# Optimization experiments

Hardware: AMD Instinct MI355X
Metric: run time of the kernel (lower is better)

The kernel has to match this reference:

```python
import jax, jax.numpy as jnp
import numpy as np
from jax import lax

B, NM, P, F, E, H, K = 32, 131072, 256, 3, 64, 4, 3
DH = E // H


def layer_norm(x, gamma, beta, eps=1e-5):
    mu = x.mean(-1, keepdims=True)
    var = ((x - mu) ** 2).mean(-1, keepdims=True)
    return (x - mu) * lax.rsqrt(var + eps) * gamma + beta


def knn_interp(x, pos_x, pos_y, k=K):
    """x: [B, Nx, F] features at pos_x [Nx, 2]; interpolate to pos_y [Ny, 2].
    Positions are shared across the batch (they are tiled in the torch code),
    so KNN indices/weights are computed once. Matches torch knn + inverse-
    squared-distance weighted scatter (uniform per-batch counts => gather form).
    """
    d2 = jnp.sum((pos_y[:, None, :] - pos_x[None, :, :]) ** 2, axis=-1)  # [Ny, Nx]
    neg_d2, idx = lax.top_k(-d2, k)                                      # [Ny, k]
    w = 1.0 / jnp.clip(-neg_d2, 1e-16)                                   # [Ny, k]
    w = lax.stop_gradient(w)  # torch computes weights under no_grad
    gathered = x[:, idx, :]                                              # [B, Ny, k, F]
    num = jnp.sum(gathered * w[None, :, :, None], axis=2)                # [B, Ny, F]
    den = jnp.sum(w, axis=1)[None, :, None]                              # [1, Ny, 1]
    return num / den


def setup_inputs() -> dict:
    key = jax.random.key(0)
    ks = jax.random.split(key, 8)
    return {
        "node_attr": jax.random.normal(ks[0], (B * NM, F), jnp.float32),
        "position_mesh": jax.random.uniform(ks[1], (NM, 2), jnp.float32),
        "position_pivotal": jax.random.uniform(ks[2], (P, 2), jnp.float32),
        "ln_gamma": jnp.ones((F,), jnp.float32),
        "ln_beta": jnp.zeros((F,), jnp.float32),
        "Wf": jax.random.normal(ks[3], (E, F), jnp.float32) * (2.0 / E) ** 0.5,
        "bf": jnp.zeros((E,), jnp.float32),
        "Wp": jax.random.normal(ks[4], (E, 2), jnp.float32) * (2.0 / E) ** 0.5,
        "bp": jnp.zeros((E,), jnp.float32),
        "in_proj_w": jax.random.normal(ks[5], (3 * E, E), jnp.float32) * (1.0 / E) ** 0.5,
        "in_proj_b": jnp.zeros((3 * E,), jnp.float32),
        "batch_size": B,
    }


def reference(node_attr, position_mesh, position_pivotal, ln_gamma, ln_beta,
              Wf, bf, Wp, bp, in_proj_w, in_proj_b, batch_size):
    x = node_attr.reshape(batch_size, -1, F)                 # [B, NM, F]
    # PivotalNorm after encoder (encoder/decoder MeshGraphNet omitted: undefined dep)
    x = layer_norm(x, ln_gamma, ln_beta)
    # ---- downsample: mesh -> pivotal via inverse-distance KNN interpolation ----
    y = knn_interp(x, position_mesh, position_pivotal)       # [B, P, F]
    # attention-based pooling over pivotal nodes
    q = (jnp.einsum('bpf,ef->bpe', y, Wf) + bf
         + (position_pivotal @ Wp.T + bp)[None])             # [B, P, E]
    Wq, Wk = in_proj_w[:E], in_proj_w[E:2 * E]
    bq, bk = in_proj_b[:E], in_proj_b[E:2 * E]
    Q = (q @ Wq.T + bq).reshape(batch_size, P, H, DH)
    Kt = (q @ Wk.T + bk).reshape(batch_size, P, H, DH)
    scores = jnp.einsum('bqhd,bkhd->bhqk', Q, Kt) / np.float32(np.sqrt(DH))
    attn = jax.nn.softmax(scores, axis=-1)                   # [B, H, P, P]
    attn_w = attn.mean(axis=1)                               # avg heads, [B, P, P]
    y = jnp.einsum('bqk,bkf->bqf', attn_w, y)                # [B, P, F]
    # ---- interpolate: pivotal -> mesh ----
    out = knn_interp(y, position_pivotal, position_mesh)     # [B, NM, F]
    return out.reshape(-1, F)
```

## Files before the change

### kernel.cpp

```cpp
#include <hip/hip_runtime.h>
#include <math.h>

#define NM 131072
#define PP 256
#define BB 32
#define INF_F 3.0e38f

#define GM   64
#define GM2  (GM * GM)
#define CAPM 96
#define GP   16
#define GP2  (GP * GP)
#define CAPP 8

typedef unsigned long long u64;

__device__ __forceinline__ u64 packkey(float d, int i) {
  return ((u64)__float_as_uint(d) << 32) | (unsigned)i;
}

__device__ __forceinline__ void ins3k(u64 k, u64& k0, u64& k1, u64& k2) {
  bool l0 = k < k0, l1 = k < k1, l2 = k < k2;
  k2 = l1 ? k1 : (l2 ? k : k2);
  k1 = l0 ? k0 : (l1 ? k : k1);
  k0 = l0 ? k : k0;
}

__device__ __forceinline__ float dist2(float ax, float ay, float bx, float by) {
  float dx = ax - bx, dy = ay - by;
  return __fadd_rn(__fmul_rn(dx, dx), __fmul_rn(dy, dy));
}

__global__ __launch_bounds__(256)
void build_buckets(const float* __restrict__ mesh, const float* __restrict__ piv,
                   unsigned* __restrict__ cntM, unsigned* __restrict__ cntP,
                   unsigned* __restrict__ ovfc,
                   float* __restrict__ bufM,
                   int* __restrict__ bufP,
                   float* __restrict__ ovfM, int* __restrict__ ovfP,
                   float* __restrict__ y2) {
  const int g = blockIdx.x * 256 + threadIdx.x;
  if (g < NM) {
    float2 mp = ((const float2*)mesh)[g];
    int cx = min((int)(mp.x * GM), GM - 1);
    int cy = min((int)(mp.y * GM), GM - 1);
    int c = cy * GM + cx;
    unsigned s = atomicAdd(&cntM[c], 1u);
    if (s < CAPM) {
      float* d = bufM + (size_t)(c * CAPM + s) * 3;
      d[0] = mp.x; d[1] = mp.y; ((int*)d)[2] = g;
    } else {
      unsigned o = atomicAdd(&ovfc[0], 1u);
      float* d = ovfM + (size_t)o * 3;
      d[0] = mp.x; d[1] = mp.y; ((int*)d)[2] = g;
    }
  }
  if (blockIdx.x == 0 && threadIdx.x < PP) {
    const int p = threadIdx.x;
    float2 pv = ((const float2*)piv)[p];
    int cx = min((int)(pv.x * GP), GP - 1);
    int cy = min((int)(pv.y * GP), GP - 1);
    int c = cy * GP + cx;
    unsigned s = atomicAdd(&cntP[c], 1u);
    if (s < CAPP) bufP[c * CAPP + s] = p;
    else { unsigned o = atomicAdd(&ovfc[1], 1u); ovfP[o] = p; }
  }
  if (blockIdx.x == 1) {
    for (int j = threadIdx.x; j < BB * PP * 3; j += 256) y2[j] = 0.f;
  }
}

__global__ __launch_bounds__(256)
void knnA_grid(const float* __restrict__ piv,
               const unsigned* __restrict__ cntM, const float* __restrict__ bufM,
               const unsigned* __restrict__ ovfc, const float* __restrict__ ovfM,
               float* __restrict__ wA, int* __restrict__ idxA) {
  const int p = blockIdx.x;
  const int t = threadIdx.x;
  __shared__ u64 sk[256 * 3];
  __shared__ u64 g3[3];
  __shared__ int sdone;

  const float2 pv = ((const float2*)piv)[p];
  const int cx = min((int)(pv.x * GM), GM - 1);
  const int cy = min((int)(pv.y * GM), GM - 1);

  u64 b0 = ~0ull, b1 = ~0ull, b2 = ~0ull;

  {
    int x0 = max(cx - 1, 0), x1 = min(cx + 1, GM - 1);
    int y0 = max(cy - 1, 0), y1 = min(cy + 1, GM - 1);
    for (int yy = y0; yy <= y1; ++yy) {
      int cb = yy * GM + x0;
      int tot = (x1 - x0 + 1) * CAPM;
      for (int s = t; s < tot; s += 256) {
        int ci = s / CAPM, j = s - ci * CAPM;
        int c = cb + ci;
        if (j < (int)min(cntM[c], (unsigned)CAPM)) {
          const float* cp = bufM + (size_t)(c * CAPM + j) * 3;
          float d = dist2(pv.x, pv.y, cp[0], cp[1]);
          ins3k(packkey(d, ((const int*)cp)[2]), b0, b1, b2);
        }
      }
    }
    int no = (int)ovfc[0];
    for (int j = t; j < no; j += 256) {
      const float* cp = ovfM + (size_t)j * 3;
      float d = dist2(pv.x, pv.y, cp[0], cp[1]);
      ins3k(packkey(d, ((const int*)cp)[2]), b0, b1, b2);
    }
  }

  int R = 1;
  u64 p0 = ~0ull, p1 = ~0ull, p2 = ~0ull;
  while (true) {
    sk[t * 3 + 0] = b0; sk[t * 3 + 1] = b1; sk[t * 3 + 2] = b2;
    __syncthreads();
    if (t < 32) {
      u64 e0 = ~0ull, e1 = ~0ull, e2 = ~0ull;
#pragma unroll
      for (int s = 0; s < 8; ++s) {
        int o = (t + 32 * s) * 3;
        ins3k(sk[o], e0, e1, e2); ins3k(sk[o + 1], e0, e1, e2); ins3k(sk[o + 2], e0, e1, e2);
      }
      sk[t * 3] = e0; sk[t * 3 + 1] = e1; sk[t * 3 + 2] = e2;
    }
    __syncthreads();
    if (t == 0) {
      u64 e0 = p0, e1 = p1, e2 = p2;
      for (int s = 0; s < 32; ++s) {
        ins3k(sk[s * 3], e0, e1, e2); ins3k(sk[s * 3 + 1], e0, e1, e2); ins3k(sk[s * 3 + 2], e0, e1, e2);
      }
      g3[0] = e0; g3[1] = e1; g3[2] = e2;
      float d2f = __uint_as_float((unsigned)(e2 >> 32));
      float md = (float)R * (1.0f / GM);
      sdone = (md * md > d2f) ? 1 : 0;
    }
    __syncthreads();
    if (sdone) break;
    p0 = g3[0]; p1 = g3[1]; p2 = g3[2];
    b0 = b1 = b2 = ~0ull;
    R += 1;
    int x0 = max(cx - R, 0), x1 = min(cx + R, GM - 1);
    for (int pass = 0; pass < 2; ++pass) {
      int yy = pass ? cy + R : cy - R;
      if (yy < 0 || yy > GM - 1) continue;
      int cb = yy * GM + x0;
      int tot = (x1 - x0 + 1) * CAPM;
      for (int s = t; s < tot; s += 256) {
        int ci = s / CAPM, j = s - ci * CAPM;
        int c = cb + ci;
        if (j < (int)min(cntM[c], (unsigned)CAPM)) {
          const float* cp = bufM + (size_t)(c * CAPM + j) * 3;
          float d = dist2(pv.x, pv.y, cp[0], cp[1]);
          ins3k(packkey(d, ((const int*)cp)[2]), b0, b1, b2);
        }
      }
    }
    int yy0 = max(cy - R + 1, 0), yy1 = min(cy + R - 1, GM - 1);
    for (int pass = 0; pass < 2; ++pass) {
      int xx = pass ? cx + R : cx - R;
      if (xx < 0 || xx > GM - 1) continue;
      int tot = (yy1 - yy0 + 1) * CAPM;
      for (int s = t; s < tot; s += 256) {
        int ri = s / CAPM, j = s - ri * CAPM;
        int c = (yy0 + ri) * GM + xx;
        if (j < (int)min(cntM[c], (unsigned)CAPM)) {
          const float* cp = bufM + (size_t)(c * CAPM + j) * 3;
          float d = dist2(pv.x, pv.y, cp[0], cp[1]);
          ins3k(packkey(d, ((const int*)cp)[2]), b0, b1, b2);
        }
      }
    }
    __syncthreads();
  }
  if (t == 0) {
#pragma unroll
    for (int k = 0; k < 3; ++k) {
      u64 e = g3[k];
      float d = __uint_as_float((unsigned)(e >> 32));
      wA[p * 3 + k] = 1.0f / fmaxf(d, 1e-16f);
      idxA[p * 3 + k] = (int)(unsigned)(e & 0xffffffffu);
    }
  }
}

__global__ __launch_bounds__(128, 2)
void gather_qqk(const float* __restrict__ node, const float* __restrict__ piv,
                const float* __restrict__ gamma, const float* __restrict__ beta,
                const float* __restrict__ Wf, const float* __restrict__ bf,
                const float* __restrict__ Wp, const float* __restrict__ bp,
                const float* __restrict__ ipw, const float* __restrict__ ipb,
                const float* __restrict__ wA, const int* __restrict__ idxA,
                float* __restrict__ y, float* __restrict__ Qh, float* __restrict__ Kh) {
  const int b = blockIdx.x >> 5;
  const int ptile = (blockIdx.x & 31) * 8;
  const int t = threadIdx.x;
  __shared__ float qs[8][64];
  __shared__ float ys[8][3];

  if (t < 8) {
    const int p = ptile + t;
    const float g0 = gamma[0], g1 = gamma[1], g2 = gamma[2];
    const float be0 = beta[0], be1 = beta[1], be2 = beta[2];
    float num0 = 0.f, num1 = 0.f, num2 = 0.f, den = 0.f;
#pragma unroll
    for (int k = 0; k < 3; ++k) {
      int idx = idxA[p * 3 + k];
      float w = wA[p * 3 + k];
      const float* r = node + ((size_t)b * NM + idx) * 3;
      float a0 = r[0], a1 = r[1], a2 = r[2];
      float mu = (a0 + a1 + a2) * (1.0f / 3.0f);
      float e0 = a0 - mu, e1 = a1 - mu, e2 = a2 - mu;
      float var = (e0 * e0 + e1 * e1 + e2 * e2) * (1.0f / 3.0f);
      float sc = 1.0f / sqrtf(var + 1e-5f);
      num0 += (e0 * sc * g0 + be0) * w;
      num1 += (e1 * sc * g1 + be1) * w;
      num2 += (e2 * sc * g2 + be2) * w;
      den += w;
    }
    float o0 = num0 / den, o1 = num1 / den, o2 = num2 / den;
    ys[t][0] = o0; ys[t][1] = o1; ys[t][2] = o2;
    float* yr = y + (b * PP + p) * 3;
    yr[0] = o0; yr[1] = o1; yr[2] = o2;
  }
  __syncthreads();

  const int e = t & 63;
  const int half = t >> 6;
  {
    float wf0 = Wf[e * 3], wf1 = Wf[e * 3 + 1], wf2 = Wf[e * 3 + 2];
    float wp0 = Wp[e * 2], wp1 = Wp[e * 2 + 1];
    float cst = bf[e] + bp[e];
    for (int r = half; r < 8; r += 2) {
      int p = ptile + r;
      float pe = piv[2 * p] * wp0 + piv[2 * p + 1] * wp1;
      qs[r][e] = ys[r][0] * wf0 + ys[r][1] * wf1 + ys[r][2] * wf2 + cst + pe;
    }
  }
  __syncthreads();

  const int row = half * 64 + e;
  float wreg[64];
  const float4* W4 = (const float4*)(ipw + row * 64);
#pragma unroll
  for (int j = 0; j < 16; ++j) {
    float4 v = W4[j];
    wreg[4 * j] = v.x; wreg[4 * j + 1] = v.y; wreg[4 * j + 2] = v.z; wreg[4 * j + 3] = v.w;
  }
  float bias = ipb[row];
  float* dst = half ? Kh : Qh;
  const int h = e >> 4, d = e & 15;
  for (int r = 0; r < 8; ++r) {
    float acc = bias;
#pragma unroll
    for (int j = 0; j < 64; ++j) acc += qs[r][j] * wreg[j];
    int p = ptile + r;
    dst[(((b * 4 + h) * PP) + p) * 16 + d] = acc;
  }
}

__global__ __launch_bounds__(256, 2)
void attn_kernel(const float* __restrict__ Qh, const float* __restrict__ Kh,
                 const float* __restrict__ y, float* __restrict__ y2) {
  const int b = blockIdx.x >> 4;
  const int h = (blockIdx.x >> 2) & 3;
  const int qq = blockIdx.x & 3;
  const int t = threadIdx.x;
  const int sub = t & 7;
  const int rt = t >> 3;

  __shared__ float4 sK[PP * 5];
  __shared__ float4 sY[PP];

  {
    const float4* src = (const float4*)(Kh + (size_t)(b * 4 + h) * PP * 16);
#pragma unroll
    for (int i = t; i < PP * 4; i += 256) {
      int k = i >> 2, j = i & 3;
      sK[k * 5 + j] = src[i];
    }
    const float* yr = y + (b * PP + t) * 3;
    sY[t] = make_float4(yr[0], yr[1], yr[2], 0.f);
  }
  __syncthreads();

  const int q0 = qq * 64 + rt * 2;
  const float4* q4 = (const float4*)(Qh + ((size_t)((b * 4 + h) * PP) + q0) * 16);
  float4 A0 = q4[0], A1 = q4[1], A2 = q4[2], A3 = q4[3];
  float4 B0 = q4[4], B1 = q4[5], B2 = q4[6], B3 = q4[7];

  float m0 = -INF_F, l0 = 0.f, x0 = 0.f, x1 = 0.f, x2 = 0.f;
  float m1 = -INF_F, l1 = 0.f, z0 = 0.f, z1 = 0.f, z2 = 0.f;

#pragma unroll 4
  for (int kk = 0; kk < 32; ++kk) {
    int k = kk * 8 + sub;
    float4 K0 = sK[k * 5 + 0], K1 = sK[k * 5 + 1], K2 = sK[k * 5 + 2], K3 = sK[k * 5 + 3];
    float4 yv = sY[k];
    float s0 = (A0.x*K0.x + A0.y*K0.y + A0.z*K0.z + A0.w*K0.w
              + A1.x*K1.x + A1.y*K1.y + A1.z*K1.z + A1.w*K1.w
              + A2.x*K2.x + A2.y*K2.y + A2.z*K2.z + A2.w*K2.w
              + A3.x*K3.x + A3.y*K3.y + A3.z*K3.z + A3.w*K3.w) * 0.25f;
    float s1 = (B0.x*K0.x + B0.y*K0.y + B0.z*K0.z + B0.w*K0.w
              + B1.x*K1.x + B1.y*K1.y + B1.z*K1.z + B1.w*K1.w
              + B2.x*K2.x + B2.y*K2.y + B2.z*K2.z + B2.w*K2.w
              + B3.x*K3.x + B3.y*K3.y + B3.z*K3.z + B3.w*K3.w) * 0.25f;
    {
      float mn = fmaxf(m0, s0);
      float p = __expf(s0 - mn), sc = __expf(m0 - mn);
      l0 = l0 * sc + p;
      x0 = x0 * sc + p * yv.x; x1 = x1 * sc + p * yv.y; x2 = x2 * sc + p * yv.z;
      m0 = mn;
    }
    {
      float mn = fmaxf(m1, s1);
      float p = __expf(s1 - mn), sc = __expf(m1 - mn);
      l1 = l1 * sc + p;
      z0 = z0 * sc + p * yv.x; z1 = z1 * sc + p * yv.y; z2 = z2 * sc + p * yv.z;
      m1 = mn;
    }
  }

#pragma unroll
  for (int off = 1; off < 8; off <<= 1) {
    float mo = __shfl_xor(m0, off), lo = __shfl_xor(l0, off);
    float b0 = __shfl_xor(x0, off), b1 = __shfl_xor(x1, off), b2 = __shfl_xor(x2, off);
    float M = fmaxf(m0, mo);
    float es = __expf(m0 - M), eo = __expf(mo - M);
    l0 = l0 * es + lo * eo;
    x0 = x0 * es + b0 * eo; x1 = x1 * es + b1 * eo; x2 = x2 * es + b2 * eo;
    m0 = M;

    float mo1 = __shfl_xor(m1, off), lo1 = __shfl_xor(l1, off);
    float c0 = __shfl_xor(z0, off), c1 = __shfl_xor(z1, off), c2 = __shfl_xor(z2, off);
    float M1 = fmaxf(m1, mo1);
    float es1 = __expf(m1 - M1), eo1 = __expf(mo1 - M1);
    l1 = l1 * es1 + lo1 * eo1;
    z0 = z0 * es1 + c0 * eo1; z1 = z1 * es1 + c1 * eo1; z2 = z2 * es1 + c2 * eo1;
    m1 = M1;
  }

  if (sub == 0) {
    float inv0 = 0.25f / l0;
    float inv1 = 0.25f / l1;
    float* o0 = y2 + (b * PP + q0) * 3;
    atomicAdd(o0 + 0, x0 * inv0);
    atomicAdd(o0 + 1, x1 * inv0);
    atomicAdd(o0 + 2, x2 * inv0);
    float* o1 = o0 + 3;
    atomicAdd(o1 + 0, z0 * inv1);
    atomicAdd(o1 + 1, z1 * inv1);
    atomicAdd(o1 + 2, z2 * inv1);
  }
}

__global__ __launch_bounds__(256)
void interp_knnB_out(const float* __restrict__ mesh, const float* __restrict__ piv,
                     const unsigned* __restrict__ cntP, const int* __restrict__ bufP,
                     const unsigned* __restrict__ ovfc, const int* __restrict__ ovfP,
                     const float* __restrict__ y2, float* __restrict__ out) {
  const int t = threadIdx.x;
  __shared__ float spx[PP], spy[PP];
  __shared__ unsigned scnt[GP2];
  __shared__ int sbuf[GP2 * CAPP];
  __shared__ float sy2[BB * PP * 3];
  {
    float2 pvv = ((const float2*)piv)[t];
    spx[t] = pvv.x; spy[t] = pvv.y;
    scnt[t] = cntP[t];
    for (int j = t; j < GP2 * CAPP; j += 256) sbuf[j] = bufP[j];
    const float4* s4 = (const float4*)y2;
    float4* d4 = (float4*)sy2;
#pragma unroll
    for (int j = t; j < BB * PP * 3 / 4; j += 256) d4[j] = s4[j];
  }
  __syncthreads();

  const int m = blockIdx.x * 256 + t;
  const float2 mv = ((const float2*)mesh)[m];
  const int cx = min((int)(mv.x * GP), GP - 1);
  const int cy = min((int)(mv.y * GP), GP - 1);
  u64 k0 = ~0ull, k1 = ~0ull, k2 = ~0ull;

  {
    int x0 = max(cx - 2, 0), x1 = min(cx + 2, GP - 1);
    int y0 = max(cy - 2, 0), y1 = min(cy + 2, GP - 1);
    for (int yy = y0; yy <= y1; ++yy)
      for (int xx = x0; xx <= x1; ++xx) {
        int c = yy * GP + xx;
        int n = (int)min(scnt[c], (unsigned)CAPP);
        for (int j = 0; j < n; ++j) {
          int qq = sbuf[c * CAPP + j];
          float d = dist2(mv.x, mv.y, spx[qq], spy[qq]);
          ins3k(packkey(d, qq), k0, k1, k2);
        }
      }
    int no = (int)ovfc[1];
    for (int j = 0; j < no; ++j) {
      int qq = ovfP[j];
      float d = dist2(mv.x, mv.y, spx[qq], spy[qq]);
      ins3k(packkey(d, qq), k0, k1, k2);
    }
  }
  int R = 2;
  while (true) {
    float d2f = __uint_as_float((unsigned)(k2 >> 32));
    float md = (float)R * (1.0f / GP);
    if (md * md > d2f) break;
    R += 1;
    if (R >= 2 * GP) break;
    int x0 = max(cx - R, 0), x1 = min(cx + R, GP - 1);
    for (int pass = 0; pass < 2; ++pass) {
      int yy = pass ? cy + R : cy - R;
      if (yy < 0 || yy > GP - 1) continue;
      for (int xx = x0; xx <= x1; ++xx) {
        int c = yy * GP + xx;
        int n = (int)min(scnt[c], (unsigned)CAPP);
        for (int j = 0; j < n; ++j) {
          int qq = sbuf[c * CAPP + j];
          float d = dist2(mv.x, mv.y, spx[qq], spy[qq]);
          ins3k(packkey(d, qq), k0, k1, k2);
        }
      }
    }
    int yy0 = max(cy - R + 1, 0), yy1 = min(cy + R - 1, GP - 1);
    for (int pass = 0; pass < 2; ++pass) {
      int xx = pass ? cx + R : cx - R;
      if (xx < 0 || xx > GP - 1) continue;
      for (int yy = yy0; yy <= yy1; ++yy) {
        int c = yy * GP + xx;
        int n = (int)min(scnt[c], (unsigned)CAPP);
        for (int j = 0; j < n; ++j) {
          int qq = sbuf[c * CAPP + j];
          float d = dist2(mv.x, mv.y, spx[qq], spy[qq]);
          ins3k(packkey(d, qq), k0, k1, k2);
        }
      }
    }
  }

  float d0 = __uint_as_float((unsigned)(k0 >> 32));
  float d1 = __uint_as_float((unsigned)(k1 >> 32));
  float d2v = __uint_as_float((unsigned)(k2 >> 32));
  int j0 = (int)(unsigned)(k0 & 0xffffffffu) * 3;
  int j1 = (int)(unsigned)(k1 & 0xffffffffu) * 3;
  int j2 = (int)(unsigned)(k2 & 0xffffffffu) * 3;
  float w0 = 1.0f / fmaxf(d0, 1e-16f);
  float w1 = 1.0f / fmaxf(d1, 1e-16f);
  float w2 = 1.0f / fmaxf(d2v, 1e-16f);
  float inv = 1.0f / (w0 + w1 + w2);

  for (int b = 0; b < BB; ++b) {
    const float* yb = sy2 + b * PP * 3;
    float r00 = yb[j0], r01 = yb[j0 + 1], r02 = yb[j0 + 2];
    float r10 = yb[j1], r11 = yb[j1 + 1], r12 = yb[j1 + 2];
    float r20 = yb[j2], r21 = yb[j2 + 1], r22 = yb[j2 + 2];
    float3 res;
    res.x = (w0 * r00 + w1 * r10 + w2 * r20) * inv;
    res.y = (w0 * r01 + w1 * r11 + w2 * r21) * inv;
    res.z = (w0 * r02 + w1 * r12 + w2 * r22) * inv;
    *(float3*)(out + ((size_t)b * NM + m) * 3) = res;
  }
}

extern "C" void kernel_launch(void* const* d_in, const int* in_sizes, int n_in,
                              void* d_out, int out_size, void* d_ws, size_t ws_size,
                              hipStream_t stream) {
  const float* node  = (const float*)d_in[0];
  const float* mesh  = (const float*)d_in[1];
  const float* piv   = (const float*)d_in[2];
  const float* gamma = (const float*)d_in[3];
  const float* beta  = (const float*)d_in[4];
  const float* Wf    = (const float*)d_in[5];
  const float* bf    = (const float*)d_in[6];
  const float* Wp    = (const float*)d_in[7];
  const float* bp    = (const float*)d_in[8];
  const float* ipw   = (const float*)d_in[9];
  const float* ipb   = (const float*)d_in[10];
  float* out = (float*)d_out;

  unsigned* cntM = (unsigned*)d_ws;
  unsigned* cntP = cntM + 4096;
  unsigned* ovfc = cntP + 256;
  float* bufM = (float*)d_ws + 4608;
  int*   bufP = (int*)(bufM + (size_t)GM2 * CAPM * 3);
  float* ovfM = (float*)(bufP + GP2 * CAPP);
  int*   ovfP = (int*)(ovfM + (size_t)NM * 3);
  float* wA   = (float*)(ovfP + PP);
  int*   idxA = (int*)(wA + PP * 3);
  float* y    = (float*)(idxA + PP * 3);
  float* Qh   = y + BB * PP * 3;
  float* Kh   = Qh + BB * PP * 64;
  float* y2   = Kh + BB * PP * 64;

  hipMemsetAsync(cntM, 0, 4608 * sizeof(unsigned), stream);
  build_buckets<<<NM / 256, 256, 0, stream>>>(mesh, piv, cntM, cntP, ovfc,
                                              bufM, bufP, ovfM, ovfP, y2);
  knnA_grid<<<PP, 256, 0, stream>>>(piv, cntM, bufM, ovfc, ovfM, wA, idxA);
  gather_qqk<<<BB * 32, 128, 0, stream>>>(node, piv, gamma, beta, Wf, bf, Wp, bp, ipw, ipb,
                                          wA, idxA, y, Qh, Kh);
  attn_kernel<<<BB * 4 * 4, 256, 0, stream>>>(Qh, Kh, y, y2);
  interp_knnB_out<<<NM / 256, 256, 0, stream>>>(mesh, piv, cntP, bufP, ovfc, ovfP, y2, out);
}
```

Before: 218.5 us.

## Drop shared y2 staging, split batch across blocks with padded float4 gathers

```diff
diff --git a/kernel.cpp b/kernel.cpp
--- a/kernel.cpp
+++ b/kernel.cpp
@@ -66,7 +66,7 @@
     else { unsigned o = atomicAdd(&ovfc[1], 1u); ovfP[o] = p; }
   }
   if (blockIdx.x == 1) {
-    for (int j = threadIdx.x; j < BB * PP * 3; j += 256) y2[j] = 0.f;
+    for (int j = threadIdx.x; j < BB * PP * 4; j += 256) y2[j] = 0.f;
   }
 }
 
@@ -344,11 +344,11 @@
   if (sub == 0) {
     float inv0 = 0.25f / l0;
     float inv1 = 0.25f / l1;
-    float* o0 = y2 + (b * PP + q0) * 3;
+    float* o0 = y2 + (size_t)(b * PP + q0) * 4;
     atomicAdd(o0 + 0, x0 * inv0);
     atomicAdd(o0 + 1, x1 * inv0);
     atomicAdd(o0 + 2, x2 * inv0);
-    float* o1 = o0 + 3;
+    float* o1 = o0 + 4;
     atomicAdd(o1 + 0, z0 * inv1);
     atomicAdd(o1 + 1, z1 * inv1);
     atomicAdd(o1 + 2, z2 * inv1);
@@ -361,23 +361,20 @@
                      const unsigned* __restrict__ ovfc, const int* __restrict__ ovfP,
                      const float* __restrict__ y2, float* __restrict__ out) {
   const int t = threadIdx.x;
+  const int mt = blockIdx.x >> 2;
+  const int bg = blockIdx.x & 3;
   __shared__ float spx[PP], spy[PP];
   __shared__ unsigned scnt[GP2];
   __shared__ int sbuf[GP2 * CAPP];
-  __shared__ float sy2[BB * PP * 3];
   {
     float2 pvv = ((const float2*)piv)[t];
     spx[t] = pvv.x; spy[t] = pvv.y;
     scnt[t] = cntP[t];
     for (int j = t; j < GP2 * CAPP; j += 256) sbuf[j] = bufP[j];
-    const float4* s4 = (const float4*)y2;
-    float4* d4 = (float4*)sy2;
-#pragma unroll
-    for (int j = t; j < BB * PP * 3 / 4; j += 256) d4[j] = s4[j];
   }
   __syncthreads();
 
-  const int m = blockIdx.x * 256 + t;
+  const int m = mt * 256 + t;
   const float2 mv = ((const float2*)mesh)[m];
   const int cx = min((int)(mv.x * GP), GP - 1);
   const int cy = min((int)(mv.y * GP), GP - 1);
@@ -443,23 +440,26 @@
   float d0 = __uint_as_float((unsigned)(k0 >> 32));
   float d1 = __uint_as_float((unsigned)(k1 >> 32));
   float d2v = __uint_as_float((unsigned)(k2 >> 32));
-  int j0 = (int)(unsigned)(k0 & 0xffffffffu) * 3;
-  int j1 = (int)(unsigned)(k1 & 0xffffffffu) * 3;
-  int j2 = (int)(unsigned)(k2 & 0xffffffffu) * 3;
+  const int j0 = (int)(unsigned)(k0 & 0xffffffffu);
+  const int j1 = (int)(unsigned)(k1 & 0xffffffffu);
+  const int j2 = (int)(unsigned)(k2 & 0xffffffffu);
   float w0 = 1.0f / fmaxf(d0, 1e-16f);
   float w1 = 1.0f / fmaxf(d1, 1e-16f);
   float w2 = 1.0f / fmaxf(d2v, 1e-16f);
   float inv = 1.0f / (w0 + w1 + w2);
 
-  for (int b = 0; b < BB; ++b) {
-    const float* yb = sy2 + b * PP * 3;
-    float r00 = yb[j0], r01 = yb[j0 + 1], r02 = yb[j0 + 2];
-    float r10 = yb[j1], r11 = yb[j1 + 1], r12 = yb[j1 + 2];
-    float r20 = yb[j2], r21 = yb[j2 + 1], r22 = yb[j2 + 2];
+  const float4* y4 = (const float4*)y2;
+#pragma unroll
+  for (int i = 0; i < 8; ++i) {
+    const int b = bg * 8 + i;
+    const int rb = b * PP;
+    float4 r0 = y4[rb + j0];
+    float4 r1 = y4[rb + j1];
+    float4 r2 = y4[rb + j2];
     float3 res;
-    res.x = (w0 * r00 + w1 * r10 + w2 * r20) * inv;
-    res.y = (w0 * r01 + w1 * r11 + w2 * r21) * inv;
-    res.z = (w0 * r02 + w1 * r12 + w2 * r22) * inv;
+    res.x = (w0 * r0.x + w1 * r1.x + w2 * r2.x) * inv;
+    res.y = (w0 * r0.y + w1 * r1.y + w2 * r2.y) * inv;
+    res.z = (w0 * r0.z + w1 * r1.z + w2 * r2.z) * inv;
     *(float3*)(out + ((size_t)b * NM + m) * 3) = res;
   }
 }
@@ -501,5 +501,5 @@
   gather_qqk<<<BB * 32, 128, 0, stream>>>(node, piv, gamma, beta, Wf, bf, Wp, bp, ipw, ipb,
                                           wA, idxA, y, Qh, Kh);
   attn_kernel<<<BB * 4 * 4, 256, 0, stream>>>(Qh, Kh, y, y2);
-  interp_knnB_out<<<NM / 256, 256, 0, stream>>>(mesh, piv, cntP, bufP, ovfc, ovfP, y2, out);
-}
+  interp_knnB_out<<<NM / 256 * 4, 256, 0, stream>>>(mesh, piv, cntP, bufP, ovfc, ovfP, y2, out);
+}
```

After: 209.8 us. 1.04x faster.
